# Kernel optimization log

Measured on AMD Instinct MI355X. Metric: run time of the kernel, lower is better.

## Reference

```python
import jax, jax.numpy as jnp
import numpy as np

EPS_NORM = 1e-12  # torch F.normalize eps


def _resize_bilinear_ac(x, H, W):
    # Bilinear resize with align_corners=True on NCHW tensor x.
    h, w = x.shape[-2], x.shape[-1]
    ys = jnp.linspace(0.0, h - 1.0, H)
    xs = jnp.linspace(0.0, w - 1.0, W)
    y0 = jnp.floor(ys).astype(jnp.int32); y1 = jnp.minimum(y0 + 1, h - 1)
    x0 = jnp.floor(xs).astype(jnp.int32); x1 = jnp.minimum(x0 + 1, w - 1)
    wy = (ys - y0).astype(x.dtype)[None, None, :, None]
    wx = (xs - x0).astype(x.dtype)
    rows = x[:, :, y0, :] * (1 - wy) + x[:, :, y1, :] * wy  # (B,C,H,w)
    return rows[:, :, :, x0] * (1 - wx) + rows[:, :, :, x1] * wx  # (B,C,H,W)


def _icc(p, b):
    # p: (b, 19, hw) row-stochastic over hw.
    # M[i, j] = KLDiv(input=p_i, target=p_j, batchmean) = (1/b) * sum p_j*(log p_j - p_i)
    # NOTE: original code passes probabilities (not log-probs) as KLDiv input; kept faithful.
    E = jnp.sum(p * jnp.log(p), axis=(0, 2))            # (19,) sum_b,k p log p
    G = jnp.einsum('bik,bjk->ij', p, p)                  # (19,19) sum_b,k p_i p_j
    M = (E[None, :] - G) / b
    sym = jnp.triu(M) + jnp.triu(M, 1).T                 # loop writes value for i<=j to both [i,j],[j,i]
    nrm = jnp.maximum(jnp.linalg.norm(sym, axis=1, keepdims=True), EPS_NORM)
    return sym / nrm                                     # F.normalize(dim=1)


def reference(s_out, t_out, t_logit, s_logit, conv_w, conv_b):
    T = 1.0  # temperature
    # --- pi_loss ---
    B, C, H, W = t_out.shape
    s1 = _resize_bilinear_ac(s_out, H, W)
    s1 = jnp.einsum('bchw,oc->bohw', s1, conv_w[:, :, 0, 0]) + conv_b[None, :, None, None]
    log_ps = jax.nn.log_softmax(s1 / T, axis=1)
    pt = jax.nn.softmax(t_out / T, axis=1)
    # torch KLDivLoss() default reduction='mean' (mean over ALL elements)
    pi_loss = jnp.mean(pt * (jnp.log(pt) - log_ps))
    # --- lo_loss ---
    b, n, h, w = s_logit.shape
    tl = _resize_bilinear_ac(t_logit, h, w)
    s = jax.nn.softmax(s_logit.reshape(b, n, h * w) / T, axis=2)
    t = jax.nn.softmax(tl.reshape(b, n, h * w) / T, axis=2)
    ICCS = _icc(s, b)
    ICCT = _icc(t, b)
    lo_loss = jnp.sum((ICCS - ICCT) ** 2)
    return pi_loss, lo_loss


def setup_inputs() -> dict:
    key = jax.random.key(0)
    k = jax.random.split(key, 6)
    return {
        's_out': jax.random.normal(k[0], (8, 128, 33, 33), jnp.float32),
        't_out': jax.random.normal(k[1], (8, 768, 65, 65), jnp.float32),
        't_logit': jax.random.normal(k[2], (8, 19, 65, 65), jnp.float32),
        's_logit': jax.random.normal(k[3], (8, 19, 129, 129), jnp.float32),
        'conv_w': jax.random.normal(k[4], (768, 128, 1, 1), jnp.float32) * 0.05,
        'conv_b': jax.random.normal(k[5], (768,), jnp.float32) * 0.05,
    }
```

## Files before the change

kernel.cpp:

```cpp
#include <hip/hip_runtime.h>
#include <math.h>

#define WS_E0   0
#define WS_E1   19
#define WS_G0   64
#define WS_G1   448
#define WS_Z    1152
#define WS_TOT  1536

typedef __bf16 bf16x8 __attribute__((ext_vector_type(8)));
typedef float  f32x4  __attribute__((ext_vector_type(4)));

__global__ void k_init(float* __restrict__ out, float* __restrict__ ws) {
    int tid = blockIdx.x * 256 + threadIdx.x;
    if (tid < 2) out[tid] = 0.f;
    if (tid < WS_TOT) ws[tid] = 0.f;
}

__launch_bounds__(256, 2)
__global__ void k_pi(const float* __restrict__ s_out, const float* __restrict__ t_out,
                     const float* __restrict__ Wg, const float* __restrict__ bias,
                     float* __restrict__ out) {
    __shared__ __align__(16) char lds[17408];
    __bf16* xs = (__bf16*)lds;
    float*  scr = (float*)lds;

    const int tid  = threadIdx.x;
    const int b    = blockIdx.x / 67;
    const int tile = blockIdx.x % 67;
    const int hw0  = tile * 64;
    const bool tail = (hw0 + 63 >= 4225);

    {
        const float* Sb = s_out + b * 128 * 1089;
        #pragma unroll
        for (int ii = 0; ii < 32; ii++) {
            int idx = tid + ii * 256;
            int c = idx >> 6, px = idx & 63;
            int hw = hw0 + px;
            float v = 0.f;
            if (hw < 4225) {
                int h = hw / 65, w = hw - h * 65;
                int y0 = h >> 1, x0 = w >> 1;
                int y1 = y0 + (h & 1), x1 = x0 + (w & 1);
                float wy = 0.5f * (float)(h & 1), wx = 0.5f * (float)(w & 1);
                const float* Sc = Sb + c * 1089;
                float v00 = Sc[y0 * 33 + x0], v01 = Sc[y0 * 33 + x1];
                float v10 = Sc[y1 * 33 + x0], v11 = Sc[y1 * 33 + x1];
                float r0 = v00 + wx * (v01 - v00);
                float r1 = v10 + wx * (v11 - v10);
                v = r0 + wy * (r1 - r0);
            }
            xs[px * 136 + c] = (__bf16)v;
        }
    }
    __syncthreads();

    const int l  = tid & 63;
    const int wv = tid >> 6;
    const int q  = l >> 4;
    const int n  = l & 15;

    bf16x8 bfrag[4][4];
    #pragma unroll
    for (int pt = 0; pt < 4; pt++)
        #pragma unroll
        for (int kf = 0; kf < 4; kf++)
            bfrag[pt][kf] = *(const bf16x8*)&xs[(pt * 16 + n) * 136 + kf * 32 + q * 8];
    __syncthreads();

    float Zt[4], St[4], Dd[4], Zs[4];
    #pragma unroll
    for (int pt = 0; pt < 4; pt++) { Zt[pt] = 0.f; St[pt] = 0.f; Dd[pt] = 0.f; Zs[pt] = 0.f; }

    for (int ch = 0; ch < 12; ch++) {
        const int ob  = ch * 64 + wv * 16;
        const int o_r = ob + q * 4;

        float tq[4][4];
        #pragma unroll
        for (int r = 0; r < 4; r++) {
            const float* trow = t_out + (b * 768 + o_r + r) * 4225;
            if (!tail) {
                #pragma unroll
                for (int pt = 0; pt < 4; pt++) tq[pt][r] = trow[hw0 + pt * 16 + n];
            } else {
                #pragma unroll
                for (int pt = 0; pt < 4; pt++) tq[pt][r] = trow[min(hw0 + pt * 16 + n, 4224)];
            }
        }
        f32x4 bq = *(const f32x4*)&bias[o_r];

        bf16x8 afrag[4];
        {
            const float* Wr = Wg + (ob + n) * 128 + q * 8;
            #pragma unroll
            for (int kf = 0; kf < 4; kf++) {
                float4 w0 = *(const float4*)&Wr[kf * 32];
                float4 w1 = *(const float4*)&Wr[kf * 32 + 4];
                bf16x8 a;
                a[0] = (__bf16)w0.x; a[1] = (__bf16)w0.y; a[2] = (__bf16)w0.z; a[3] = (__bf16)w0.w;
                a[4] = (__bf16)w1.x; a[5] = (__bf16)w1.y; a[6] = (__bf16)w1.z; a[7] = (__bf16)w1.w;
                afrag[kf] = a;
            }
        }

        f32x4 acc[4];
        #pragma unroll
        for (int pt = 0; pt < 4; pt++) {
            f32x4 a0 = {0.f, 0.f, 0.f, 0.f};
            #pragma unroll
            for (int kf = 0; kf < 4; kf++)
                a0 = __builtin_amdgcn_mfma_f32_16x16x32_bf16(afrag[kf], bfrag[pt][kf], a0, 0, 0, 0);
            acc[pt] = a0;
        }

        #pragma unroll
        for (int pt = 0; pt < 4; pt++) {
            #pragma unroll
            for (int r = 0; r < 4; r++) {
                float s1v = acc[pt][r] + bq[r];
                float tv  = tq[pt][r];
                float e   = __expf(tv);
                Zt[pt] += e;
                St[pt]  = fmaf(e, tv,  St[pt]);
                Dd[pt]  = fmaf(e, s1v, Dd[pt]);
                Zs[pt] += __expf(s1v);
            }
        }
    }

    __syncthreads();
    {
        int part = wv * 4 + q;
        #pragma unroll
        for (int pt = 0; pt < 4; pt++) {
            f32x4 v = {Zt[pt], St[pt], Dd[pt], Zs[pt]};
            *(f32x4*)&scr[(pt * 16 + n) * 68 + part * 4] = v;
        }
    }
    __syncthreads();
    if (tid < 64) {
        float Z = 0.f, S = 0.f, D = 0.f, Z2 = 0.f;
        #pragma unroll
        for (int p = 0; p < 16; p++) {
            const float* s4 = &scr[tid * 68 + p * 4];
            Z += s4[0]; S += s4[1]; D += s4[2]; Z2 += s4[3];
        }
        float contrib = (S - D) / Z - logf(Z) + logf(Z2);
        if (hw0 + tid >= 4225) contrib = 0.f;
        for (int off = 32; off > 0; off >>= 1) contrib += __shfl_down(contrib, off);
        if (tid == 0) atomicAdd(out, contrib * (1.0f / 25958400.0f));
    }
}

__device__ __forceinline__ float t_resized(const float* __restrict__ Trow, int k) {
    int y = k / 129, x = k - y * 129;
    int y0 = y >> 1, x0 = x >> 1;
    int y1 = y0 + (y & 1), x1 = x0 + (x & 1);
    float fy = 0.5f * (float)(y & 1), fx = 0.5f * (float)(x & 1);
    float v00 = Trow[y0 * 65 + x0], v01 = Trow[y0 * 65 + x1];
    float v10 = Trow[y1 * 65 + x0], v11 = Trow[y1 * 65 + x1];
    float r0 = v00 + fx * (v01 - v00);
    float r1 = v10 + fx * (v11 - v10);
    return r0 + fy * (r1 - r0);
}

__global__ void k_rowstats(const float* __restrict__ s_logit, const float* __restrict__ t_logit,
                           float* __restrict__ ws) {
    __shared__ float red[8];
    int row  = blockIdx.x;
    int side = (row >= 152) ? 1 : 0;
    int r    = side ? row - 152 : row;
    const float* src = side ? (t_logit + r * 4225) : (s_logit + r * 16641);
    int tid = threadIdx.x;

    float z = 0.f, s = 0.f;
    for (int k = tid; k < 16641; k += 256) {
        float v = side ? t_resized(src, k) : src[k];
        float e = __expf(v);
        z += e;
        s = fmaf(e, v, s);
    }
    for (int off = 32; off > 0; off >>= 1) { z += __shfl_down(z, off); s += __shfl_down(s, off); }
    if ((tid & 63) == 0) { red[tid >> 6] = z; red[4 + (tid >> 6)] = s; }
    __syncthreads();
    if (tid == 0) {
        float Z = red[0] + red[1] + red[2] + red[3];
        float S = red[4] + red[5] + red[6] + red[7];
        ws[WS_Z + row] = Z;
        int nn = r % 19;
        atomicAdd(&ws[(side ? WS_E1 : WS_E0) + nn], S / Z - logf(Z));
    }
}

#define KT 512
#define KP 516
__global__ void k_gram(const float* __restrict__ s_logit, const float* __restrict__ t_logit,
                       float* __restrict__ ws) {
    __shared__ float pbuf[19 * KP];
    __shared__ float rowiz[19];
    int blk  = blockIdx.x;
    int side = (blk >= 264) ? 1 : 0;
    int rm   = side ? blk - 264 : blk;
    int b = rm / 33, kt = rm % 33;
    int k0 = kt * KT;
    int tid = threadIdx.x;

    if (tid < 19) {
        int row = side * 152 + b * 19 + tid;
        rowiz[tid] = 1.0f / ws[WS_Z + row];
    }
    __syncthreads();

    for (int i = 0; i < 19; i++) {
        const float* src = side ? (t_logit + (b * 19 + i) * 4225) : (s_logit + (b * 19 + i) * 16641);
        float iz = rowiz[i];
        for (int kl = tid; kl < KT; kl += 256) {
            int k = k0 + kl;
            float p = 0.f;
            if (k < 16641) {
                float v = side ? t_resized(src, k) : src[k];
                p = __expf(v) * iz;
            }
            pbuf[i * KP + kl] = p;
        }
    }
    __syncthreads();

    if (tid < 190) {
        int t = tid, i = 0;
        while (t >= 19 - i) { t -= 19 - i; i++; }
        int j = i + t;
        const float* pi_ = &pbuf[i * KP];
        const float* pj_ = &pbuf[j * KP];
        float g = 0.f;
        #pragma unroll 4
        for (int kl = 0; kl < KT; kl += 4) {
            float4 a = *(const float4*)&pi_[kl];
            float4 c = *(const float4*)&pj_[kl];
            g = fmaf(a.x, c.x, g); g = fmaf(a.y, c.y, g);
            g = fmaf(a.z, c.z, g); g = fmaf(a.w, c.w, g);
        }
        atomicAdd(&ws[(side ? WS_G1 : WS_G0) + i * 19 + j], g);
    }
}

__global__ void k_final(const float* __restrict__ ws, float* __restrict__ out) {
    __shared__ float Ms[361], Mt[361], ns[19], nt[19];
    __shared__ float red[8];
    int tid = threadIdx.x;
    if (tid < 361) {
        int i = tid / 19, j = tid - i * 19;
        int lo = min(i, j), hi = max(i, j);
        Ms[tid] = (ws[WS_E0 + hi] - ws[WS_G0 + lo * 19 + hi]) * 0.125f;
        Mt[tid] = (ws[WS_E1 + hi] - ws[WS_G1 + lo * 19 + hi]) * 0.125f;
    }
    __syncthreads();
    if (tid < 19) {
        float as = 0.f, at = 0.f;
        for (int j = 0; j < 19; j++) {
            as = fmaf(Ms[tid * 19 + j], Ms[tid * 19 + j], as);
            at = fmaf(Mt[tid * 19 + j], Mt[tid * 19 + j], at);
        }
        ns[tid] = fmaxf(sqrtf(as), 1e-12f);
        nt[tid] = fmaxf(sqrtf(at), 1e-12f);
    }
    __syncthreads();
    float d = 0.f;
    if (tid < 361) {
        int i = tid / 19;
        float v = Ms[tid] / ns[i] - Mt[tid] / nt[i];
        d = v * v;
    }
    for (int off = 32; off > 0; off >>= 1) d += __shfl_down(d, off);
    if ((tid & 63) == 0) red[tid >> 6] = d;
    __syncthreads();
    if (tid == 0) out[1] = red[0] + red[1] + red[2] + red[3] + red[4] + red[5];
}

extern "C" void kernel_launch(void* const* d_in, const int* in_sizes, int n_in,
                              void* d_out, int out_size, void* d_ws, size_t ws_size,
                              hipStream_t stream) {
    const float* s_out   = (const float*)d_in[0];
    const float* t_out   = (const float*)d_in[1];
    const float* t_logit = (const float*)d_in[2];
    const float* s_logit = (const float*)d_in[3];
    const float* conv_w  = (const float*)d_in[4];
    const float* conv_b  = (const float*)d_in[5];
    float* out = (float*)d_out;
    float* ws  = (float*)d_ws;

    k_init<<<dim3(6), dim3(256), 0, stream>>>(out, ws);
    k_pi<<<dim3(536), dim3(256), 0, stream>>>(s_out, t_out, conv_w, conv_b, out);
    k_rowstats<<<dim3(304), dim3(256), 0, stream>>>(s_logit, t_logit, ws);
    k_gram<<<dim3(528), dim3(256), 0, stream>>>(s_logit, t_logit, ws);
    k_final<<<dim3(1), dim3(384), 0, stream>>>(ws, out);
}
```

Measured before the change: 290.9 us.

## Fuse pi and rowstats kernels, split channels, prefetch t_out, precast weights

Conv weights are cast to bf16 once in the init kernel instead of per block and per chunk. The pi kernel is merged with rowstats into one launch, and the pi work is split into two halves over output channels to double the block count. t_out loads become float4-vectorised and are staged through LDS with a one-chunk register prefetch. Per-pixel partial stats go to workspace and are reduced later in the gram kernel launch, trading extra workspace traffic and more register pressure for more parallelism and overlap.

```diff
diff --git a/kernel.cpp b/kernel.cpp
--- a/kernel.cpp
+++ b/kernel.cpp
@@ -6,151 +6,25 @@
 #define WS_G0   64
 #define WS_G1   448
 #define WS_Z    1152
-#define WS_TOT  1536
+#define WS_WBF  2048
+#define WS_PIX  51200
+#define PIXHALF 137216
 
 typedef __bf16 bf16x8 __attribute__((ext_vector_type(8)));
 typedef float  f32x4  __attribute__((ext_vector_type(4)));
 
-__global__ void k_init(float* __restrict__ out, float* __restrict__ ws) {
-    int tid = blockIdx.x * 256 + threadIdx.x;
-    if (tid < 2) out[tid] = 0.f;
-    if (tid < WS_TOT) ws[tid] = 0.f;
-}
-
-__launch_bounds__(256, 2)
-__global__ void k_pi(const float* __restrict__ s_out, const float* __restrict__ t_out,
-                     const float* __restrict__ Wg, const float* __restrict__ bias,
-                     float* __restrict__ out) {
-    __shared__ __align__(16) char lds[17408];
-    __bf16* xs = (__bf16*)lds;
-    float*  scr = (float*)lds;
-
-    const int tid  = threadIdx.x;
-    const int b    = blockIdx.x / 67;
-    const int tile = blockIdx.x % 67;
-    const int hw0  = tile * 64;
-    const bool tail = (hw0 + 63 >= 4225);
-
-    {
-        const float* Sb = s_out + b * 128 * 1089;
-        #pragma unroll
-        for (int ii = 0; ii < 32; ii++) {
-            int idx = tid + ii * 256;
-            int c = idx >> 6, px = idx & 63;
-            int hw = hw0 + px;
-            float v = 0.f;
-            if (hw < 4225) {
-                int h = hw / 65, w = hw - h * 65;
-                int y0 = h >> 1, x0 = w >> 1;
-                int y1 = y0 + (h & 1), x1 = x0 + (w & 1);
-                float wy = 0.5f * (float)(h & 1), wx = 0.5f * (float)(w & 1);
-                const float* Sc = Sb + c * 1089;
-                float v00 = Sc[y0 * 33 + x0], v01 = Sc[y0 * 33 + x1];
-                float v10 = Sc[y1 * 33 + x0], v11 = Sc[y1 * 33 + x1];
-                float r0 = v00 + wx * (v01 - v00);
-                float r1 = v10 + wx * (v11 - v10);
-                v = r0 + wy * (r1 - r0);
-            }
-            xs[px * 136 + c] = (__bf16)v;
-        }
-    }
-    __syncthreads();
-
-    const int l  = tid & 63;
-    const int wv = tid >> 6;
-    const int q  = l >> 4;
-    const int n  = l & 15;
-
-    bf16x8 bfrag[4][4];
+__global__ void k_init(const float* __restrict__ conv_w, float* __restrict__ ws,
+                       float* __restrict__ out) {
+    int gid = blockIdx.x * 256 + threadIdx.x;
+    __bf16* Wb = (__bf16*)(ws + WS_WBF);
     #pragma unroll
-    for (int pt = 0; pt < 4; pt++)
-        #pragma unroll
-        for (int kf = 0; kf < 4; kf++)
-            bfrag[pt][kf] = *(const bf16x8*)&xs[(pt * 16 + n) * 136 + kf * 32 + q * 8];
-    __syncthreads();
-
-    float Zt[4], St[4], Dd[4], Zs[4];
-    #pragma unroll
-    for (int pt = 0; pt < 4; pt++) { Zt[pt] = 0.f; St[pt] = 0.f; Dd[pt] = 0.f; Zs[pt] = 0.f; }
-
-    for (int ch = 0; ch < 12; ch++) {
-        const int ob  = ch * 64 + wv * 16;
-        const int o_r = ob + q * 4;
-
-        float tq[4][4];
-        #pragma unroll
-        for (int r = 0; r < 4; r++) {
-            const float* trow = t_out + (b * 768 + o_r + r) * 4225;
-            if (!tail) {
-                #pragma unroll
-                for (int pt = 0; pt < 4; pt++) tq[pt][r] = trow[hw0 + pt * 16 + n];
-            } else {
-                #pragma unroll
-                for (int pt = 0; pt < 4; pt++) tq[pt][r] = trow[min(hw0 + pt * 16 + n, 4224)];
-            }
-        }
-        f32x4 bq = *(const f32x4*)&bias[o_r];
-
-        bf16x8 afrag[4];
-        {
-            const float* Wr = Wg + (ob + n) * 128 + q * 8;
-            #pragma unroll
-            for (int kf = 0; kf < 4; kf++) {
-                float4 w0 = *(const float4*)&Wr[kf * 32];
-                float4 w1 = *(const float4*)&Wr[kf * 32 + 4];
-                bf16x8 a;
-                a[0] = (__bf16)w0.x; a[1] = (__bf16)w0.y; a[2] = (__bf16)w0.z; a[3] = (__bf16)w0.w;
-                a[4] = (__bf16)w1.x; a[5] = (__bf16)w1.y; a[6] = (__bf16)w1.z; a[7] = (__bf16)w1.w;
-                afrag[kf] = a;
-            }
-        }
-
-        f32x4 acc[4];
-        #pragma unroll
-        for (int pt = 0; pt < 4; pt++) {
-            f32x4 a0 = {0.f, 0.f, 0.f, 0.f};
-            #pragma unroll
-            for (int kf = 0; kf < 4; kf++)
-                a0 = __builtin_amdgcn_mfma_f32_16x16x32_bf16(afrag[kf], bfrag[pt][kf], a0, 0, 0, 0);
-            acc[pt] = a0;
-        }
-
-        #pragma unroll
-        for (int pt = 0; pt < 4; pt++) {
-            #pragma unroll
-            for (int r = 0; r < 4; r++) {
-                float s1v = acc[pt][r] + bq[r];
-                float tv  = tq[pt][r];
-                float e   = __expf(tv);
-                Zt[pt] += e;
-                St[pt]  = fmaf(e, tv,  St[pt]);
-                Dd[pt]  = fmaf(e, s1v, Dd[pt]);
-                Zs[pt] += __expf(s1v);
-            }
-        }
-    }
-
-    __syncthreads();
-    {
-        int part = wv * 4 + q;
-        #pragma unroll
-        for (int pt = 0; pt < 4; pt++) {
-            f32x4 v = {Zt[pt], St[pt], Dd[pt], Zs[pt]};
-            *(f32x4*)&scr[(pt * 16 + n) * 68 + part * 4] = v;
-        }
-    }
-    __syncthreads();
-    if (tid < 64) {
-        float Z = 0.f, S = 0.f, D = 0.f, Z2 = 0.f;
-        #pragma unroll
-        for (int p = 0; p < 16; p++) {
-            const float* s4 = &scr[tid * 68 + p * 4];
-            Z += s4[0]; S += s4[1]; D += s4[2]; Z2 += s4[3];
-        }
-        float contrib = (S - D) / Z - logf(Z) + logf(Z2);
-        if (hw0 + tid >= 4225) contrib = 0.f;
-        for (int off = 32; off > 0; off >>= 1) contrib += __shfl_down(contrib, off);
-        if (tid == 0) atomicAdd(out, contrib * (1.0f / 25958400.0f));
+    for (int j = 0; j < 6; j++) {
+        int idx = gid + j * 16384;
+        Wb[idx] = (__bf16)conv_w[idx];
+    }
+    if (blockIdx.x == 0) {
+        for (int k = (int)threadIdx.x; k < 2048; k += 256) ws[k] = 0.f;
+        if (threadIdx.x < 2) out[threadIdx.x] = 0.f;
     }
 }
 
@@ -166,83 +40,255 @@
     return r0 + fy * (r1 - r0);
 }
 
-__global__ void k_rowstats(const float* __restrict__ s_logit, const float* __restrict__ t_logit,
-                           float* __restrict__ ws) {
-    __shared__ float red[8];
-    int row  = blockIdx.x;
-    int side = (row >= 152) ? 1 : 0;
-    int r    = side ? row - 152 : row;
-    const float* src = side ? (t_logit + r * 4225) : (s_logit + r * 16641);
-    int tid = threadIdx.x;
-
-    float z = 0.f, s = 0.f;
-    for (int k = tid; k < 16641; k += 256) {
-        float v = side ? t_resized(src, k) : src[k];
-        float e = __expf(v);
-        z += e;
-        s = fmaf(e, v, s);
-    }
-    for (int off = 32; off > 0; off >>= 1) { z += __shfl_down(z, off); s += __shfl_down(s, off); }
-    if ((tid & 63) == 0) { red[tid >> 6] = z; red[4 + (tid >> 6)] = s; }
-    __syncthreads();
-    if (tid == 0) {
-        float Z = red[0] + red[1] + red[2] + red[3];
-        float S = red[4] + red[5] + red[6] + red[7];
-        ws[WS_Z + row] = Z;
-        int nn = r % 19;
-        atomicAdd(&ws[(side ? WS_E1 : WS_E0) + nn], S / Z - logf(Z));
+__launch_bounds__(256, 4)
+__global__ void k_main(const float* __restrict__ s_out, const float* __restrict__ t_out,
+                       const float* __restrict__ bias,
+                       const float* __restrict__ s_logit, const float* __restrict__ t_logit,
+                       float* __restrict__ ws, float* __restrict__ out) {
+    __shared__ __align__(16) char lds[17408];
+    const int tid = threadIdx.x;
+    const int bx  = blockIdx.x;
+
+    if (bx < 1072) {
+        __bf16* xs    = (__bf16*)lds;
+        float*  tbase = (float*)lds;
+        float*  scr   = (float*)lds;
+
+        const int half = bx & 1;
+        const int bt   = bx >> 1;
+        const int b    = bt / 67;
+        const int tile = bt - b * 67;
+        const int hw0  = tile * 64;
+        const bool tail = (tile == 66);
+
+        {
+            const float* Sb = s_out + b * 128 * 1089;
+            #pragma unroll
+            for (int ii = 0; ii < 32; ii++) {
+                int idx = tid + ii * 256;
+                int c = idx >> 6, px = idx & 63;
+                int hw = hw0 + px;
+                float v = 0.f;
+                if (hw < 4225) {
+                    int h = hw / 65, w = hw - h * 65;
+                    int y0 = h >> 1, x0 = w >> 1;
+                    int y1 = y0 + (h & 1), x1 = x0 + (w & 1);
+                    float wy = 0.5f * (float)(h & 1), wx = 0.5f * (float)(w & 1);
+                    const float* Sc = Sb + c * 1089;
+                    float v00 = Sc[y0 * 33 + x0], v01 = Sc[y0 * 33 + x1];
+                    float v10 = Sc[y1 * 33 + x0], v11 = Sc[y1 * 33 + x1];
+                    float r0 = v00 + wx * (v01 - v00);
+                    float r1 = v10 + wx * (v11 - v10);
+                    v = r0 + wy * (r1 - r0);
+                }
+                xs[px * 136 + c] = (__bf16)v;
+            }
+        }
+        __syncthreads();
+
+        const int l = tid & 63, wv = tid >> 6, q = l >> 4, n = l & 15;
+
+        bf16x8 bfrag[4][4];
+        #pragma unroll
+        for (int pt = 0; pt < 4; pt++)
+            #pragma unroll
+            for (int kf = 0; kf < 4; kf++)
+                bfrag[pt][kf] = *(const bf16x8*)&xs[(pt * 16 + n) * 136 + kf * 32 + q * 8];
+        __syncthreads();
+
+        const __bf16* Wbf = (const __bf16*)(ws + WS_WBF);
+        float* tst = tbase + wv * 1088;
+
+        float Zt[4], St[4], Dd[4], Zs[4];
+        #pragma unroll
+        for (int pt = 0; pt < 4; pt++) { Zt[pt] = 0.f; St[pt] = 0.f; Dd[pt] = 0.f; Zs[pt] = 0.f; }
+
+        float4 t4[4];
+        auto load_t = [&](int ch, float4* dst) {
+            const float* tb = t_out + (size_t)(b * 768 + ch * 64 + wv * 16) * 4225;
+            #pragma unroll
+            for (int ii = 0; ii < 4; ii++) {
+                int lin = ii * 64 + l;
+                int row = lin >> 4, p4 = lin & 15;
+                if (!tail) {
+                    dst[ii] = *(const float4*)(tb + row * 4225 + hw0 + p4 * 4);
+                } else {
+                    const float* rr = tb + row * 4225;
+                    int b0 = hw0 + p4 * 4;
+                    float4 v;
+                    v.x = rr[min(b0 + 0, 4224)];
+                    v.y = rr[min(b0 + 1, 4224)];
+                    v.z = rr[min(b0 + 2, 4224)];
+                    v.w = rr[min(b0 + 3, 4224)];
+                    dst[ii] = v;
+                }
+            }
+        };
+        load_t(half * 6, t4);
+
+        for (int c6 = 0; c6 < 6; c6++) {
+            const int ch  = half * 6 + c6;
+            const int ob  = ch * 64 + wv * 16;
+            const int o_r = ob + q * 4;
+
+            #pragma unroll
+            for (int ii = 0; ii < 4; ii++) {
+                int lin = ii * 64 + l;
+                int row = lin >> 4, p4 = lin & 15;
+                *(float4*)(tst + row * 68 + p4 * 4) = t4[ii];
+            }
+
+            bf16x8 afrag[4];
+            const __bf16* Wr = Wbf + (size_t)(ob + n) * 128 + q * 8;
+            #pragma unroll
+            for (int kf = 0; kf < 4; kf++)
+                afrag[kf] = *(const bf16x8*)(Wr + kf * 32);
+            f32x4 bq = *(const f32x4*)&bias[o_r];
+
+            float4 t4n[4];
+            const bool pf = (c6 < 5);
+            if (pf) load_t(ch + 1, t4n);
+
+            f32x4 acc[4];
+            #pragma unroll
+            for (int pt = 0; pt < 4; pt++) {
+                f32x4 a0 = {0.f, 0.f, 0.f, 0.f};
+                #pragma unroll
+                for (int kf = 0; kf < 4; kf++)
+                    a0 = __builtin_amdgcn_mfma_f32_16x16x32_bf16(afrag[kf], bfrag[pt][kf], a0, 0, 0, 0);
+                acc[pt] = a0;
+            }
+
+            #pragma unroll
+            for (int pt = 0; pt < 4; pt++) {
+                #pragma unroll
+                for (int r = 0; r < 4; r++) {
+                    float tv  = tst[(q * 4 + r) * 68 + pt * 16 + n];
+                    float s1v = acc[pt][r] + bq[r];
+                    float e   = __expf(tv);
+                    Zt[pt] += e;
+                    St[pt]  = fmaf(e, tv,  St[pt]);
+                    Dd[pt]  = fmaf(e, s1v, Dd[pt]);
+                    Zs[pt] += __expf(s1v);
+                }
+            }
+
+            if (pf) {
+                #pragma unroll
+                for (int ii = 0; ii < 4; ii++) t4[ii] = t4n[ii];
+            }
+        }
+
+        __syncthreads();
+        {
+            int part = wv * 4 + q;
+            #pragma unroll
+            for (int pt = 0; pt < 4; pt++) {
+                f32x4 v = {Zt[pt], St[pt], Dd[pt], Zs[pt]};
+                *(f32x4*)&scr[(pt * 16 + n) * 68 + part * 4] = v;
+            }
+        }
+        __syncthreads();
+        if (tid < 64) {
+            float Z = 0.f, S = 0.f, D = 0.f, Z2 = 0.f;
+            #pragma unroll
+            for (int p = 0; p < 16; p++) {
+                const float* s4 = &scr[tid * 68 + p * 4];
+                Z += s4[0]; S += s4[1]; D += s4[2]; Z2 += s4[3];
+            }
+            f32x4 v = {Z, S, D, Z2};
+            *(f32x4*)&ws[WS_PIX + half * PIXHALF + ((size_t)b * 4288 + tile * 64 + tid) * 4] = v;
+        }
+    } else {
+        float* red = (float*)lds;
+        int row  = bx - 1072;
+        int side = (row >= 152) ? 1 : 0;
+        int r    = side ? row - 152 : row;
+        const float* src = side ? (t_logit + r * 4225) : (s_logit + r * 16641);
+
+        float z = 0.f, s = 0.f;
+        for (int k = tid; k < 16641; k += 256) {
+            float v = side ? t_resized(src, k) : src[k];
+            float e = __expf(v);
+            z += e;
+            s = fmaf(e, v, s);
+        }
+        for (int off = 32; off > 0; off >>= 1) { z += __shfl_down(z, off); s += __shfl_down(s, off); }
+        if ((tid & 63) == 0) { red[tid >> 6] = z; red[4 + (tid >> 6)] = s; }
+        __syncthreads();
+        if (tid == 0) {
+            float Z = red[0] + red[1] + red[2] + red[3];
+            float S = red[4] + red[5] + red[6] + red[7];
+            ws[WS_Z + row] = Z;
+            atomicAdd(&ws[(side ? WS_E1 : WS_E0) + (r % 19)], S / Z - logf(Z));
+        }
     }
 }
 
 #define KT 512
 #define KP 516
-__global__ void k_gram(const float* __restrict__ s_logit, const float* __restrict__ t_logit,
-                       float* __restrict__ ws) {
-    __shared__ float pbuf[19 * KP];
-    __shared__ float rowiz[19];
-    int blk  = blockIdx.x;
-    int side = (blk >= 264) ? 1 : 0;
-    int rm   = side ? blk - 264 : blk;
-    int b = rm / 33, kt = rm % 33;
-    int k0 = kt * KT;
-    int tid = threadIdx.x;
-
-    if (tid < 19) {
-        int row = side * 152 + b * 19 + tid;
-        rowiz[tid] = 1.0f / ws[WS_Z + row];
-    }
-    __syncthreads();
-
-    for (int i = 0; i < 19; i++) {
-        const float* src = side ? (t_logit + (b * 19 + i) * 4225) : (s_logit + (b * 19 + i) * 16641);
-        float iz = rowiz[i];
-        for (int kl = tid; kl < KT; kl += 256) {
-            int k = k0 + kl;
-            float p = 0.f;
-            if (k < 16641) {
-                float v = side ? t_resized(src, k) : src[k];
-                p = __expf(v) * iz;
-            }
-            pbuf[i * KP + kl] = p;
-        }
-    }
-    __syncthreads();
-
-    if (tid < 190) {
-        int t = tid, i = 0;
-        while (t >= 19 - i) { t -= 19 - i; i++; }
-        int j = i + t;
-        const float* pi_ = &pbuf[i * KP];
-        const float* pj_ = &pbuf[j * KP];
-        float g = 0.f;
-        #pragma unroll 4
-        for (int kl = 0; kl < KT; kl += 4) {
-            float4 a = *(const float4*)&pi_[kl];
-            float4 c = *(const float4*)&pj_[kl];
-            g = fmaf(a.x, c.x, g); g = fmaf(a.y, c.y, g);
-            g = fmaf(a.z, c.z, g); g = fmaf(a.w, c.w, g);
-        }
-        atomicAdd(&ws[(side ? WS_G1 : WS_G0) + i * 19 + j], g);
+__global__ void k_mid(const float* __restrict__ s_logit, const float* __restrict__ t_logit,
+                      float* __restrict__ ws, float* __restrict__ out) {
+    __shared__ __align__(16) char lds[39296];
+    const int tid = threadIdx.x;
+    const int bx  = blockIdx.x;
+
+    if (bx < 528) {
+        float* pbuf  = (float*)lds;
+        float* rowiz = (float*)(lds + 39216);
+        int side = (bx >= 264) ? 1 : 0;
+        int rm   = side ? bx - 264 : bx;
+        int b = rm / 33, kt = rm - b * 33;
+        int k0 = kt * KT;
+
+        if (tid < 19) rowiz[tid] = 1.0f / ws[WS_Z + side * 152 + b * 19 + tid];
+        __syncthreads();
+
+        for (int i = 0; i < 19; i++) {
+            const float* src = side ? (t_logit + (b * 19 + i) * 4225) : (s_logit + (b * 19 + i) * 16641);
+            float iz = rowiz[i];
+            for (int kl = tid; kl < KT; kl += 256) {
+                int k = k0 + kl;
+                float p = 0.f;
+                if (k < 16641) {
+                    float v = side ? t_resized(src, k) : src[k];
+                    p = __expf(v) * iz;
+                }
+                pbuf[i * KP + kl] = p;
+            }
+        }
+        __syncthreads();
+
+        if (tid < 190) {
+            int t = tid, i = 0;
+            while (t >= 19 - i) { t -= 19 - i; i++; }
+            int j = i + t;
+            const float* pi_ = &pbuf[i * KP];
+            const float* pj_ = &pbuf[j * KP];
+            float g = 0.f;
+            #pragma unroll 4
+            for (int kl = 0; kl < KT; kl += 4) {
+                float4 a = *(const float4*)&pi_[kl];
+                float4 c = *(const float4*)&pj_[kl];
+                g = fmaf(a.x, c.x, g); g = fmaf(a.y, c.y, g);
+                g = fmaf(a.z, c.z, g); g = fmaf(a.w, c.w, g);
+            }
+            atomicAdd(&ws[(side ? WS_G1 : WS_G0) + i * 19 + j], g);
+        }
+    } else {
+        float* red = (float*)lds;
+        int gp = (bx - 528) * 256 + tid;
+        int b  = gp / 4288;
+        int tp = gp - b * 4288;
+        f32x4 a = *(const f32x4*)&ws[WS_PIX + (size_t)gp * 4];
+        f32x4 c = *(const f32x4*)&ws[WS_PIX + PIXHALF + (size_t)gp * 4];
+        float Z = a[0] + c[0], S = a[1] + c[1], D = a[2] + c[2], Z2 = a[3] + c[3];
+        float contrib = (tp < 4225) ? ((S - D) / Z - logf(Z) + logf(Z2)) : 0.f;
+        for (int off = 32; off > 0; off >>= 1) contrib += __shfl_down(contrib, off);
+        if ((tid & 63) == 0) red[tid >> 6] = contrib;
+        __syncthreads();
+        if (tid == 0)
+            atomicAdd(out, (red[0] + red[1] + red[2] + red[3]) * (1.0f / 25958400.0f));
     }
 }
 
@@ -291,9 +337,8 @@
     float* out = (float*)d_out;
     float* ws  = (float*)d_ws;
 
-    k_init<<<dim3(6), dim3(256), 0, stream>>>(out, ws);
-    k_pi<<<dim3(536), dim3(256), 0, stream>>>(s_out, t_out, conv_w, conv_b, out);
-    k_rowstats<<<dim3(304), dim3(256), 0, stream>>>(s_logit, t_logit, ws);
-    k_gram<<<dim3(528), dim3(256), 0, stream>>>(s_logit, t_logit, ws);
+    k_init<<<dim3(64), dim3(256), 0, stream>>>(conv_w, ws, out);
+    k_main<<<dim3(1376), dim3(256), 0, stream>>>(s_out, t_out, conv_b, s_logit, t_logit, ws, out);
+    k_mid<<<dim3(662), dim3(256), 0, stream>>>(s_logit, t_logit, ws, out);
     k_final<<<dim3(1), dim3(384), 0, stream>>>(ws, out);
 }
```

After: 304.9 us. 1.05x slower.
